# Kernel optimization log

Hardware: AMD Instinct MI355X
Metric: run time of the kernel (lower is better)

The kernel has to match this reference:

```python
import jax, jax.numpy as jnp
import numpy as np

B, D, E = 65536, 1024, 16
H1, H2 = 128, 64          # expert hidden dims (hidden_dim=128, hidden_dim//2)
R1, R2 = 64, 32           # router hidden dims
EPS = 1e-5                # BatchNorm eps


def setup_inputs() -> dict:
    key = jax.random.key(0)
    ks = jax.random.split(key, 16)
    s = 0.02
    inp = {
        "x": jax.random.normal(ks[0], (B, D), jnp.float32),
        # router BatchNorm1d (eval mode: running stats)
        "r_gamma": jnp.ones((D,), jnp.float32),
        "r_beta": jnp.zeros((D,), jnp.float32),
        "r_mean": jnp.zeros((D,), jnp.float32),
        "r_var": jnp.ones((D,), jnp.float32),
        # router MLP D->64->32->16
        "rW1": jax.random.normal(ks[1], (D, R1), jnp.float32) * s,
        "rb1": jnp.full((R1,), 0.1, jnp.float32),
        "rW2": jax.random.normal(ks[2], (R1, R2), jnp.float32) * s,
        "rb2": jnp.full((R2,), 0.1, jnp.float32),
        "rW3": jax.random.normal(ks[3], (R2, E), jnp.float32) * s,
        "rb3": jnp.full((E,), 0.1, jnp.float32),
        # per-expert BatchNorm1d (eval mode)
        "e_gamma": jnp.ones((E, D), jnp.float32),
        "e_beta": jnp.zeros((E, D), jnp.float32),
        "e_mean": jnp.zeros((E, D), jnp.float32),
        "e_var": jnp.ones((E, D), jnp.float32),
        # per-expert MLP D->128->64->1, stacked along expert dim
        "eW1": jax.random.normal(ks[4], (E, D, H1), jnp.float32) * s,
        "eb1": jnp.full((E, H1), 0.1, jnp.float32),
        "eW2": jax.random.normal(ks[5], (E, H1, H2), jnp.float32) * s,
        "eb2": jnp.full((E, H2), 0.1, jnp.float32),
        "eW3": jax.random.normal(ks[6], (E, H2, 1), jnp.float32) * s,
        "eb3": jnp.full((E, 1), 0.1, jnp.float32),
    }
    return inp


def reference(x, r_gamma, r_beta, r_mean, r_var, rW1, rb1, rW2, rb2, rW3, rb3,
              e_gamma, e_beta, e_mean, e_var, eW1, eb1, eW2, eb2, eW3, eb3):
    # ---- router: BN (eval) -> Linear/ReLU -> Linear/ReLU -> Linear -> softmax
    xn = (x - r_mean) * (r_gamma / jnp.sqrt(r_var + EPS)) + r_beta   # [B,D]
    h = jax.nn.relu(xn @ rW1 + rb1)
    h = jax.nn.relu(h @ rW2 + rb2)
    routing_weights = jax.nn.softmax(h @ rW3 + rb3, axis=1)          # [B,E]

    # ---- experts: fold per-expert BN into first linear to avoid [E,B,D] copy
    scale = e_gamma / jnp.sqrt(e_var + EPS)                          # [E,D]
    shift = e_beta - e_mean * scale                                  # [E,D]
    W1_eff = eW1 * scale[:, :, None]                                 # [E,D,H1]
    b1_eff = eb1 + jnp.einsum('ed,edh->eh', shift, eW1)              # [E,H1]

    h1 = jax.nn.relu(jnp.einsum('bd,edh->ebh', x, W1_eff) + b1_eff[:, None, :])  # [E,B,H1]
    h2 = jax.nn.relu(jnp.einsum('ebh,ehk->ebk', h1, eW2) + eb2[:, None, :])      # [E,B,H2]
    logits = jnp.einsum('ebk,eko->ebo', h2, eW3) + eb3[:, None, :]               # [E,B,1]
    expert_outputs = jax.nn.sigmoid(logits[:, :, 0]).T               # [B,E]

    weighted_pred = jnp.sum(routing_weights * expert_outputs, axis=1)  # [B]
    return weighted_pred, routing_weights, expert_outputs
```

## Files before the change

### kernel.cpp

```cpp
#include <hip/hip_runtime.h>


typedef unsigned short u16;
typedef __attribute__((ext_vector_type(8))) short bf16x8;
typedef __attribute__((ext_vector_type(4))) float f32x4;
typedef __attribute__((ext_vector_type(8))) unsigned short u16x8;
typedef __attribute__((ext_vector_type(4))) unsigned short u16x4;

#define MFMA16(a, b, c) __builtin_amdgcn_mfma_f32_16x16x32_bf16(a, b, c, 0, 0, 0)

#define B_ROWS 65536
#define NE 16
#define EPS 1e-5f

#define SBAR() __builtin_amdgcn_s_barrier()
#define VMCNT(n)                                             \
    do {                                                     \
        asm volatile("s_waitcnt vmcnt(" #n ")" ::: "memory");\
        __builtin_amdgcn_sched_barrier(0);                   \
    } while (0)

__device__ inline u16 f2bf(float f) {
    union { float f; unsigned u; } c; c.f = f;
    unsigned u = c.u;
    return (u16)((u + 0x7fffu + ((u >> 16) & 1u)) >> 16);
}

__device__ inline void gload16(const u16* g, u16* s) {
    __builtin_amdgcn_global_load_lds(
        (const __attribute__((address_space(1))) unsigned int*)g,
        (__attribute__((address_space(3))) unsigned int*)s,
        16, 0, 0);
}


__device__ void body_prep_x(int blk, int tid, const float* __restrict__ x,
                            u16* __restrict__ xs_g, u16* __restrict__ lds) {
    int p = tid & 15, rloc = tid >> 4;
    int r_g = blk * 16 + rloc;
    int lb = p & 7;
    int swz = (rloc >> 1) & 3;
    const float* xrow = x + (size_t)r_g * 1024;
#pragma unroll
    for (int i = 0; i < 8; ++i) {
        int kc = 2 * i + (p >> 3);
        int c = kc * 64 + lb * 8;
        float4 f0 = *(const float4*)(xrow + c);
        float4 f1 = *(const float4*)(xrow + c + 4);
        u16x8 u;
        u[0] = f2bf(f0.x); u[1] = f2bf(f0.y); u[2] = f2bf(f0.z); u[3] = f2bf(f0.w);
        u[4] = f2bf(f1.x); u[5] = f2bf(f1.y); u[6] = f2bf(f1.z); u[7] = f2bf(f1.w);
        int s = c >> 5;
        int q = (c >> 3) & 3;
        *(u16x8*)&lds[s * 512 + rloc * 32 + ((q ^ swz) << 3)] = u;
    }
    __syncthreads();
    int rb = blk >> 4, m0 = (blk & 15) * 16;
    int lane = tid & 63, th = tid >> 6;
#pragma unroll
    for (int j = 0; j < 8; ++j) {
        int c = j * 4 + th;
        u16x8 v = *(const u16x8*)&lds[c * 512 + lane * 8];
        *(u16x8*)&xs_g[((size_t)(rb * 32 + c) << 13) + m0 * 32 + lane * 8] = v;
    }
}

__device__ void body_prep_w1s(int t, const float* __restrict__ eW1, const float* __restrict__ eg,
                              const float* __restrict__ ev, u16* __restrict__ w1s) {
    int qp = t & 3, h = (t >> 2) & 255, s = (t >> 10) & 31, nt = t >> 15;
    int q = qp ^ ((h >> 1) & 3);
    int e = nt * 2 + (h >> 7), hl = h & 127;
    int k0 = s * 32 + q * 8;
    u16x8 u;
#pragma unroll
    for (int j = 0; j < 8; ++j) {
        int d = k0 + j;
        float sc = eg[e * 1024 + d] * rsqrtf(ev[e * 1024 + d] + EPS);
        u[j] = f2bf(eW1[((size_t)e * 1024 + d) * 128 + hl] * sc);
    }
    *(u16x8*)&w1s[((size_t)(nt * 32 + s) << 13) + h * 32 + qp * 8] = u;
}

__device__ void body_prep_b1(int g, int lane, const float* __restrict__ eW1,
                             const float* __restrict__ eg, const float* __restrict__ eb,
                             const float* __restrict__ em, const float* __restrict__ ev,
                             const float* __restrict__ eb1, float* __restrict__ b1e) {
    int e = g >> 7, h = g & 127;
    float s = 0.f;
    for (int d = lane; d < 1024; d += 64) {
        float sc = eg[e * 1024 + d] * rsqrtf(ev[e * 1024 + d] + EPS);
        float sh = eb[e * 1024 + d] - em[e * 1024 + d] * sc;
        s += sh * eW1[((size_t)e * 1024 + d) * 128 + h];
    }
#pragma unroll
    for (int m = 1; m < 64; m <<= 1) s += __shfl_xor(s, m, 64);
    if (lane == 0) b1e[e * 128 + h] = eb1[e * 128 + h] + s;
}

__device__ void body_prep_rw1s(int t, const float* __restrict__ rW1, const float* __restrict__ rg,
                               const float* __restrict__ rv, u16* __restrict__ rw1s) {
    int qp = t & 3, jj = (t >> 2) & 63, s = t >> 8;
    int q = qp ^ ((jj >> 1) & 3);
    int k0 = s * 32 + q * 8;
    u16x8 u;
#pragma unroll
    for (int k = 0; k < 8; ++k) {
        int d = k0 + k;
        float sc = rg[d] * rsqrtf(rv[d] + EPS);
        u[k] = f2bf(rW1[d * 64 + jj] * sc);
    }
    *(u16x8*)&rw1s[(s << 11) + jj * 32 + qp * 8] = u;
}

__device__ void body_prep_rb1(int j, int lane, const float* __restrict__ rW1,
                              const float* __restrict__ rg, const float* __restrict__ rbta,
                              const float* __restrict__ rm, const float* __restrict__ rv,
                              const float* __restrict__ rb1, float* __restrict__ rb1e) {
    float s = 0.f;
    for (int d = lane; d < 1024; d += 64) {
        float sc = rg[d] * rsqrtf(rv[d] + EPS);
        float sh = rbta[d] - rm[d] * sc;
        s += sh * rW1[d * 64 + j];
    }
#pragma unroll
    for (int m = 1; m < 64; m <<= 1) s += __shfl_xor(s, m, 64);
    if (lane == 0) rb1e[j] = rb1[j] + s;
}

__device__ void body_prep_w2s(int t, const float* __restrict__ eW2, u16* __restrict__ w2s) {
    int p = t & 15, j = (t >> 4) & 63, e = t >> 10;
    int lb = p ^ (j & 7);
    int h0 = lb * 8;
    u16x8 u;
#pragma unroll
    for (int jj = 0; jj < 8; ++jj)
        u[jj] = f2bf(eW2[((size_t)e * 128 + h0 + jj) * 64 + j]);
    *(u16x8*)&w2s[((e * 64 + j) << 7) + p * 8] = u;
}

__global__ __launch_bounds__(256) void prep_all(
    const float* __restrict__ x, u16* __restrict__ xs_g,
    const float* __restrict__ eW1, const float* __restrict__ eg,
    const float* __restrict__ eb, const float* __restrict__ em,
    const float* __restrict__ ev, const float* __restrict__ eb1,
    u16* __restrict__ w1s, float* __restrict__ b1e,
    const float* __restrict__ rW1, const float* __restrict__ rg,
    const float* __restrict__ rbta, const float* __restrict__ rm,
    const float* __restrict__ rv, const float* __restrict__ rb1,
    u16* __restrict__ rw1s, float* __restrict__ rb1e,
    const float* __restrict__ eW2, u16* __restrict__ w2s) {
    __shared__ __align__(16) u16 lds[16384];
    int bid = blockIdx.x, tid = threadIdx.x;
    if (bid < 4096) {
        body_prep_x(bid, tid, x, xs_g, lds);
    } else if (bid < 5120) {
        body_prep_w1s((bid - 4096) * 256 + tid, eW1, eg, ev, w1s);
    } else if (bid < 5632) {
        body_prep_b1((bid - 5120) * 4 + (tid >> 6), tid & 63, eW1, eg, eb, em, ev, eb1, b1e);
    } else if (bid < 5664) {
        body_prep_rw1s((bid - 5632) * 256 + tid, rW1, rg, rv, rw1s);
    } else if (bid < 5680) {
        body_prep_rb1((bid - 5664) * 4 + (tid >> 6), tid & 63, rW1, rg, rbta, rm, rv, rb1, rb1e);
    } else {
        body_prep_w2s((bid - 5680) * 256 + tid, eW2, w2s);
    }
}

__global__ __launch_bounds__(512, 2) void fused_main(
    const u16* __restrict__ xs_g, const u16* __restrict__ w1s,
    const float* __restrict__ b1e, const u16* __restrict__ w2s,
    const float* __restrict__ eb2, const float* __restrict__ eW3,
    const float* __restrict__ eb3, float* __restrict__ out_eo,
    const u16* __restrict__ rw1s, const float* __restrict__ rb1e,
    const float* __restrict__ rW2, const float* __restrict__ rb2,
    const float* __restrict__ rW3, const float* __restrict__ rb3,
    float* __restrict__ out_rw) {
    __shared__ __align__(16) char smem[131072];

    int tid = threadIdx.x;
    int wave = tid >> 6, lane = tid & 63, quad = lane >> 4, l15 = lane & 15;
    int phq = (quad ^ ((l15 >> 1) & 3)) * 8;

    if (blockIdx.x >= 256) {
        int i = blockIdx.x - 256;
        int rb = (i & 7) * 32 + ((i >> 3) >> 3);
        int nt = (i >> 3) & 7;
        int wm = wave >> 2, wn = wave & 3;

        u16* ring = (u16*)smem;
        const u16* gA = w1s + ((size_t)nt << 18);
        const u16* gB = xs_g + ((size_t)rb << 18);

        f32x4 acc[8][4] = {};

        auto STAGE = [&](int t) {
            u16* ls = ring + (t & 3) * 16384 + wave * 1024;
            const u16* ga = gA + (t << 13) + wave * 1024;
            const u16* gb = gB + (t << 13) + wave * 1024;
            gload16(ga + lane * 8, ls);
            gload16(ga + 512 + lane * 8, ls + 512);
            gload16(gb + lane * 8, ls + 8192);
            gload16(gb + 512 + lane * 8, ls + 8192 + 512);
        };
        auto COMPUTE = [&](int t) {
            const u16* lA = ring + (t & 3) * 16384;
            const u16* lB = lA + 8192;
            bf16x8 a[8], b[4];
#pragma unroll
            for (int ii = 0; ii < 8; ++ii)
                a[ii] = *(const bf16x8*)&lA[(wm * 128 + ii * 16 + l15) * 32 + phq];
#pragma unroll
            for (int jj = 0; jj < 4; ++jj)
                b[jj] = *(const bf16x8*)&lB[(wn * 64 + jj * 16 + l15) * 32 + phq];
            __builtin_amdgcn_s_setprio(1);
#pragma unroll
            for (int ii = 0; ii < 8; ++ii)
#pragma unroll
                for (int jj = 0; jj < 4; ++jj)
                    acc[ii][jj] = MFMA16(a[ii], b[jj], acc[ii][jj]);
            __builtin_amdgcn_s_setprio(0);
        };

        STAGE(0); STAGE(1); STAGE(2);
#pragma clang loop unroll(disable)
        for (int s = 0; s < 29; ++s) {
            SBAR();
            STAGE(s + 3);
            VMCNT(12);
            SBAR();
            COMPUTE(s);
        }
        SBAR(); VMCNT(8); SBAR(); COMPUTE(29);
        SBAR(); VMCNT(4); SBAR(); COMPUTE(30);
        SBAR(); VMCNT(0); SBAR(); COMPUTE(31);

        int e = nt * 2 + wm;
        u16* h1 = ring;
        SBAR();
#pragma unroll
        for (int ii = 0; ii < 8; ++ii) {
            float4 bv = *(const float4*)&b1e[e * 128 + ii * 16 + quad * 4];
            float bva[4] = {bv.x, bv.y, bv.z, bv.w};
            int h0 = wm * 128 + ii * 16 + quad * 4;
            int oc = h0 >> 3, hin = h0 & 7;
#pragma unroll
            for (int jj = 0; jj < 4; ++jj) {
                int m = wn * 64 + jj * 16 + l15;
                u16x4 pk;
#pragma unroll
                for (int r = 0; r < 4; ++r)
                    pk[r] = f2bf(fmaxf(acc[ii][jj][r] + bva[r], 0.f));
                int poc = (oc & 24) | ((oc ^ m) & 7);
                *(u16x4*)&h1[m * 256 + poc * 8 + hin] = pk;
            }
        }
        bf16x8 w2f[4][4];
        const u16* gW2 = w2s + e * 8192;
#pragma unroll
        for (int ks = 0; ks < 4; ++ks)
#pragma unroll
            for (int tj = 0; tj < 4; ++tj) {
                int jc = tj * 16 + l15;
                int pq = (ks * 4 + quad) ^ (jc & 7);
                w2f[ks][tj] = *(const bf16x8*)&gW2[jc * 128 + pq * 8];
            }
        asm volatile("s_waitcnt lgkmcnt(0)" ::: "memory");
        __builtin_amdgcn_sched_barrier(0);
        SBAR();

        f32x4 acc2[4][4] = {};
#pragma unroll
        for (int ks = 0; ks < 4; ++ks) {
            bf16x8 a2[4];
#pragma unroll
            for (int mi = 0; mi < 4; ++mi) {
                int m = wn * 64 + mi * 16 + l15;
                int oc2 = wm * 16 + ks * 4 + quad;
                int poc2 = (oc2 & 24) | ((oc2 ^ m) & 7);
                a2[mi] = *(const bf16x8*)&h1[m * 256 + poc2 * 8];
            }
#pragma unroll
            for (int mi = 0; mi < 4; ++mi)
#pragma unroll
                for (int tj = 0; tj < 4; ++tj)
                    acc2[mi][tj] = MFMA16(a2[mi], w2f[ks][tj], acc2[mi][tj]);
        }

        float b2v[4], w3v[4];
#pragma unroll
        for (int tj = 0; tj < 4; ++tj) {
            int jc = tj * 16 + l15;
            b2v[tj] = eb2[e * 64 + jc];
            w3v[tj] = eW3[e * 64 + jc];
        }
        float be3 = eb3[e];
#pragma unroll
        for (int mi = 0; mi < 4; ++mi) {
            float sv[4] = {0.f, 0.f, 0.f, 0.f};
#pragma unroll
            for (int tj = 0; tj < 4; ++tj)
#pragma unroll
                for (int r = 0; r < 4; ++r)
                    sv[r] += fmaxf(acc2[mi][tj][r] + b2v[tj], 0.f) * w3v[tj];
#pragma unroll
            for (int mask = 1; mask < 16; mask <<= 1)
#pragma unroll
                for (int r = 0; r < 4; ++r) sv[r] += __shfl_xor(sv[r], mask, 64);
            if (l15 == 0) {
#pragma unroll
                for (int r = 0; r < 4; ++r) {
                    int m = wn * 64 + mi * 16 + quad * 4 + r;
                    float z = sv[r] + be3;
                    out_eo[(size_t)(rb * 256 + m) * 16 + e] = 1.f / (1.f + __expf(-z));
                }
            }
        }
    } else {
        int rb = blockIdx.x;
        u16* ldsX = (u16*)smem;
        u16* ldsW = (u16*)smem + 16384;
        float* h_r = (float*)smem;
        float* h2s = (float*)(smem + 69632);
        const u16* gB = xs_g + ((size_t)rb << 18);

        f32x4 accr[4][2] = {};
        for (int kt = 0; kt < 16; ++kt) {
            const u16* gx = gB + ((size_t)(2 * kt) << 13) + wave * 1024;
            const u16* gw = rw1s + ((2 * kt) << 11) + wave * 512;
            u16* lx = ldsX + wave * 1024;
            gload16(gx + lane * 8, lx);
            gload16(gx + 512 + lane * 8, lx + 512);
            gload16(gx + 8192 + lane * 8, lx + 8192);
            gload16(gx + 8192 + 512 + lane * 8, lx + 8192 + 512);
            gload16(gw + lane * 8, ldsW + wave * 512);
            __syncthreads();
#pragma unroll
            for (int st = 0; st < 2; ++st) {
                bf16x8 aw[4], bx[2];
#pragma unroll
                for (int jf = 0; jf < 4; ++jf)
                    aw[jf] = *(const bf16x8*)&ldsW[st * 2048 + (jf * 16 + l15) * 32 + phq];
#pragma unroll
                for (int mf = 0; mf < 2; ++mf)
                    bx[mf] = *(const bf16x8*)&ldsX[st * 8192 + (wave * 32 + mf * 16 + l15) * 32 + phq];
#pragma unroll
                for (int jf = 0; jf < 4; ++jf)
#pragma unroll
                    for (int mf = 0; mf < 2; ++mf)
                        accr[jf][mf] = MFMA16(aw[jf], bx[mf], accr[jf][mf]);
            }
            __syncthreads();
        }

#pragma unroll
        for (int jf = 0; jf < 4; ++jf) {
            int j0 = jf * 16 + quad * 4;
            float4 bv = *(const float4*)&rb1e[j0];
#pragma unroll
            for (int mf = 0; mf < 2; ++mf) {
                int m = wave * 32 + mf * 16 + l15;
                float4 hv;
                hv.x = fmaxf(accr[jf][mf][0] + bv.x, 0.f);
                hv.y = fmaxf(accr[jf][mf][1] + bv.y, 0.f);
                hv.z = fmaxf(accr[jf][mf][2] + bv.z, 0.f);
                hv.w = fmaxf(accr[jf][mf][3] + bv.w, 0.f);
                *(float4*)&h_r[m * 68 + j0] = hv;
            }
        }
        __syncthreads();

        {
            int m = tid & 255, qg = tid >> 8;
            float h2r[16];
#pragma unroll
            for (int k = 0; k < 16; ++k) h2r[k] = 0.f;
            for (int i2 = 0; i2 < 64; ++i2) {
                float hv = h_r[m * 68 + i2];
                const float4* wrow = (const float4*)&rW2[i2 * 32 + qg * 16];
                float w[16];
                *(float4*)&w[0] = wrow[0];
                *(float4*)&w[4] = wrow[1];
                *(float4*)&w[8] = wrow[2];
                *(float4*)&w[12] = wrow[3];
#pragma unroll
                for (int k = 0; k < 16; ++k) h2r[k] += hv * w[k];
            }
#pragma unroll
            for (int k = 0; k < 16; ++k)
                h2r[k] = fmaxf(h2r[k] + rb2[qg * 16 + k], 0.f);
#pragma unroll
            for (int k = 0; k < 16; k += 4)
                *(float4*)&h2s[m * 36 + qg * 16 + k] = *(float4*)&h2r[k];
        }
        __syncthreads();

        if (tid < 256) {
            int mm = tid;
            float lg[16];
#pragma unroll
            for (int o = 0; o < 16; ++o) lg[o] = 0.f;
            for (int q = 0; q < 32; ++q) {
                float hv = h2s[mm * 36 + q];
                const float4* wr = (const float4*)&rW3[q * 16];
                float w[16];
                *(float4*)&w[0] = wr[0];
                *(float4*)&w[4] = wr[1];
                *(float4*)&w[8] = wr[2];
                *(float4*)&w[12] = wr[3];
#pragma unroll
                for (int o = 0; o < 16; ++o) lg[o] += hv * w[o];
            }
#pragma unroll
            for (int o = 0; o < 16; ++o) lg[o] += rb3[o];
            float mx = lg[0];
#pragma unroll
            for (int o = 1; o < 16; ++o) mx = fmaxf(mx, lg[o]);
            float ss = 0.f;
#pragma unroll
            for (int o = 0; o < 16; ++o) { lg[o] = __expf(lg[o] - mx); ss += lg[o]; }
            float inv = 1.f / ss;
            size_t base = (size_t)(rb * 256 + mm) * 16;
#pragma unroll
            for (int o = 0; o < 16; o += 4) {
                float4 v;
                v.x = lg[o] * inv; v.y = lg[o + 1] * inv;
                v.z = lg[o + 2] * inv; v.w = lg[o + 3] * inv;
                *(float4*)&out_rw[base + o] = v;
            }
        }
    }
}

__global__ void combine_kernel(const float* __restrict__ rw, const float* __restrict__ eo,
                               float* __restrict__ wp) {
    int b = blockIdx.x * 256 + threadIdx.x;
    const float4* r4 = (const float4*)(rw + (size_t)b * 16);
    const float4* o4 = (const float4*)(eo + (size_t)b * 16);
    float s = 0.f;
#pragma unroll
    for (int k = 0; k < 4; ++k) {
        float4 r = r4[k], o = o4[k];
        s += r.x * o.x + r.y * o.y + r.z * o.z + r.w * o.w;
    }
    wp[b] = s;
}


extern "C" void kernel_launch(void* const* d_in, const int* in_sizes, int n_in,
                              void* d_out, int out_size, void* d_ws, size_t ws_size,
                              hipStream_t stream) {
    const float* x       = (const float*)d_in[0];
    const float* r_gamma = (const float*)d_in[1];
    const float* r_beta  = (const float*)d_in[2];
    const float* r_mean  = (const float*)d_in[3];
    const float* r_var   = (const float*)d_in[4];
    const float* rW1     = (const float*)d_in[5];
    const float* rb1     = (const float*)d_in[6];
    const float* rW2     = (const float*)d_in[7];
    const float* rb2     = (const float*)d_in[8];
    const float* rW3     = (const float*)d_in[9];
    const float* rb3     = (const float*)d_in[10];
    const float* e_gamma = (const float*)d_in[11];
    const float* e_beta  = (const float*)d_in[12];
    const float* e_mean  = (const float*)d_in[13];
    const float* e_var   = (const float*)d_in[14];
    const float* eW1     = (const float*)d_in[15];
    const float* eb1     = (const float*)d_in[16];
    const float* eW2     = (const float*)d_in[17];
    const float* eb2     = (const float*)d_in[18];
    const float* eW3     = (const float*)d_in[19];
    const float* eb3     = (const float*)d_in[20];

    char* ws = (char*)d_ws;
    u16* xs_g   = (u16*)ws;
    u16* w1s    = (u16*)(ws + 134217728);
    u16* rw1s   = (u16*)(ws + 138412032);
    u16* w2s    = (u16*)(ws + 138543104);
    float* b1e  = (float*)(ws + 138805248);
    float* rb1e = (float*)(ws + 138813440);

    float* out_wp = (float*)d_out;
    float* out_rw = out_wp + B_ROWS;
    float* out_eo = out_rw + (size_t)B_ROWS * NE;

    prep_all<<<5744, 256, 0, stream>>>(
        x, xs_g,
        eW1, e_gamma, e_beta, e_mean, e_var, eb1, w1s, b1e,
        rW1, r_gamma, r_beta, r_mean, r_var, rb1, rw1s, rb1e,
        eW2, w2s);

    fused_main<<<2304, 512, 0, stream>>>(
        xs_g, w1s, b1e, w2s, eb2, eW3, eb3, out_eo,
        rw1s, rb1e, rW2, rb2, rW3, rb3, out_rw);

    combine_kernel<<<256, 256, 0, stream>>>(out_rw, out_eo, out_wp);
}
```

Before: 731.3 us.

## Use row-major bf16 operands and double-buffer MFMA fragments in expert GEMM loop

The prep kernel now writes x and the folded W1 matrices as plain row-major bf16, replacing the pre-tiled, swizzled layouts, which removes the LDS transpose pass in x prep. The main kernel gathers 32-wide K slices straight from the row-major arrays and drops the XOR swizzle on LDS reads. The K loop is restructured so register fragments for the next stage load while the current stage's MFMAs run (ping-pong fa0/fa1), and it waits with a different vmcnt. Dropping the swizzle risks LDS bank conflicts, and the strided global gathers may coalesce less well.

After: 748.8 us. 1.02x slower.

```diff
diff --git a/kernel.cpp b/kernel.cpp
--- a/kernel.cpp
+++ b/kernel.cpp
@@ -35,50 +35,32 @@
 
 
 __device__ void body_prep_x(int blk, int tid, const float* __restrict__ x,
-                            u16* __restrict__ xs_g, u16* __restrict__ lds) {
-    int p = tid & 15, rloc = tid >> 4;
-    int r_g = blk * 16 + rloc;
-    int lb = p & 7;
-    int swz = (rloc >> 1) & 3;
-    const float* xrow = x + (size_t)r_g * 1024;
+                            u16* __restrict__ xbf) {
 #pragma unroll
     for (int i = 0; i < 8; ++i) {
-        int kc = 2 * i + (p >> 3);
-        int c = kc * 64 + lb * 8;
-        float4 f0 = *(const float4*)(xrow + c);
-        float4 f1 = *(const float4*)(xrow + c + 4);
+        size_t fi = (((size_t)blk * 2048) + i * 256 + tid) * 8;
+        float4 f0 = *(const float4*)(x + fi);
+        float4 f1 = *(const float4*)(x + fi + 4);
         u16x8 u;
         u[0] = f2bf(f0.x); u[1] = f2bf(f0.y); u[2] = f2bf(f0.z); u[3] = f2bf(f0.w);
         u[4] = f2bf(f1.x); u[5] = f2bf(f1.y); u[6] = f2bf(f1.z); u[7] = f2bf(f1.w);
-        int s = c >> 5;
-        int q = (c >> 3) & 3;
-        *(u16x8*)&lds[s * 512 + rloc * 32 + ((q ^ swz) << 3)] = u;
-    }
-    __syncthreads();
-    int rb = blk >> 4, m0 = (blk & 15) * 16;
-    int lane = tid & 63, th = tid >> 6;
+        *(u16x8*)&xbf[fi] = u;
+    }
+}
+
+__device__ void body_prep_w1s(int t, const float* __restrict__ eW1, const float* __restrict__ eg,
+                              const float* __restrict__ ev, u16* __restrict__ w1sr) {
+    int ko = t & 127, h = t >> 7;
+    int nt = h >> 8, sub = h & 255;
+    int e = nt * 2 + (sub >> 7), hl = sub & 127;
+    u16x8 u;
 #pragma unroll
     for (int j = 0; j < 8; ++j) {
-        int c = j * 4 + th;
-        u16x8 v = *(const u16x8*)&lds[c * 512 + lane * 8];
-        *(u16x8*)&xs_g[((size_t)(rb * 32 + c) << 13) + m0 * 32 + lane * 8] = v;
-    }
-}
-
-__device__ void body_prep_w1s(int t, const float* __restrict__ eW1, const float* __restrict__ eg,
-                              const float* __restrict__ ev, u16* __restrict__ w1s) {
-    int qp = t & 3, h = (t >> 2) & 255, s = (t >> 10) & 31, nt = t >> 15;
-    int q = qp ^ ((h >> 1) & 3);
-    int e = nt * 2 + (h >> 7), hl = h & 127;
-    int k0 = s * 32 + q * 8;
-    u16x8 u;
-#pragma unroll
-    for (int j = 0; j < 8; ++j) {
-        int d = k0 + j;
+        int d = ko * 8 + j;
         float sc = eg[e * 1024 + d] * rsqrtf(ev[e * 1024 + d] + EPS);
         u[j] = f2bf(eW1[((size_t)e * 1024 + d) * 128 + hl] * sc);
     }
-    *(u16x8*)&w1s[((size_t)(nt * 32 + s) << 13) + h * 32 + qp * 8] = u;
+    *(u16x8*)&w1sr[((size_t)h << 10) + ko * 8] = u;
 }
 
 __device__ void body_prep_b1(int g, int lane, const float* __restrict__ eW1,
@@ -98,18 +80,16 @@
 }
 
 __device__ void body_prep_rw1s(int t, const float* __restrict__ rW1, const float* __restrict__ rg,
-                               const float* __restrict__ rv, u16* __restrict__ rw1s) {
-    int qp = t & 3, jj = (t >> 2) & 63, s = t >> 8;
-    int q = qp ^ ((jj >> 1) & 3);
-    int k0 = s * 32 + q * 8;
+                               const float* __restrict__ rv, u16* __restrict__ rw1sr) {
+    int ko = t & 127, j = t >> 7;
     u16x8 u;
 #pragma unroll
     for (int k = 0; k < 8; ++k) {
-        int d = k0 + k;
+        int d = ko * 8 + k;
         float sc = rg[d] * rsqrtf(rv[d] + EPS);
-        u[k] = f2bf(rW1[d * 64 + jj] * sc);
-    }
-    *(u16x8*)&rw1s[(s << 11) + jj * 32 + qp * 8] = u;
+        u[k] = f2bf(rW1[d * 64 + j] * sc);
+    }
+    *(u16x8*)&rw1sr[(j << 10) + ko * 8] = u;
 }
 
 __device__ void body_prep_rb1(int j, int lane, const float* __restrict__ rW1,
@@ -139,26 +119,25 @@
 }
 
 __global__ __launch_bounds__(256) void prep_all(
-    const float* __restrict__ x, u16* __restrict__ xs_g,
+    const float* __restrict__ x, u16* __restrict__ xbf,
     const float* __restrict__ eW1, const float* __restrict__ eg,
     const float* __restrict__ eb, const float* __restrict__ em,
     const float* __restrict__ ev, const float* __restrict__ eb1,
-    u16* __restrict__ w1s, float* __restrict__ b1e,
+    u16* __restrict__ w1sr, float* __restrict__ b1e,
     const float* __restrict__ rW1, const float* __restrict__ rg,
     const float* __restrict__ rbta, const float* __restrict__ rm,
     const float* __restrict__ rv, const float* __restrict__ rb1,
-    u16* __restrict__ rw1s, float* __restrict__ rb1e,
+    u16* __restrict__ rw1sr, float* __restrict__ rb1e,
     const float* __restrict__ eW2, u16* __restrict__ w2s) {
-    __shared__ __align__(16) u16 lds[16384];
     int bid = blockIdx.x, tid = threadIdx.x;
     if (bid < 4096) {
-        body_prep_x(bid, tid, x, xs_g, lds);
+        body_prep_x(bid, tid, x, xbf);
     } else if (bid < 5120) {
-        body_prep_w1s((bid - 4096) * 256 + tid, eW1, eg, ev, w1s);
+        body_prep_w1s((bid - 4096) * 256 + tid, eW1, eg, ev, w1sr);
     } else if (bid < 5632) {
         body_prep_b1((bid - 5120) * 4 + (tid >> 6), tid & 63, eW1, eg, eb, em, ev, eb1, b1e);
     } else if (bid < 5664) {
-        body_prep_rw1s((bid - 5632) * 256 + tid, rW1, rg, rv, rw1s);
+        body_prep_rw1s((bid - 5632) * 256 + tid, rW1, rg, rv, rw1sr);
     } else if (bid < 5680) {
         body_prep_rb1((bid - 5664) * 4 + (tid >> 6), tid & 63, rW1, rg, rbta, rm, rv, rb1, rb1e);
     } else {
@@ -167,11 +146,11 @@
 }
 
 __global__ __launch_bounds__(512, 2) void fused_main(
-    const u16* __restrict__ xs_g, const u16* __restrict__ w1s,
+    const u16* __restrict__ xbf, const u16* __restrict__ w1sr,
     const float* __restrict__ b1e, const u16* __restrict__ w2s,
     const float* __restrict__ eb2, const float* __restrict__ eW3,
     const float* __restrict__ eb3, float* __restrict__ out_eo,
-    const u16* __restrict__ rw1s, const float* __restrict__ rb1e,
+    const u16* __restrict__ rw1sr, const float* __restrict__ rb1e,
     const float* __restrict__ rW2, const float* __restrict__ rb2,
     const float* __restrict__ rW3, const float* __restrict__ rb3,
     float* __restrict__ out_rw) {
@@ -179,60 +158,89 @@
 
     int tid = threadIdx.x;
     int wave = tid >> 6, lane = tid & 63, quad = lane >> 4, l15 = lane & 15;
-    int phq = (quad ^ ((l15 >> 1) & 3)) * 8;
+    int lr = lane >> 2, lc = lane & 3;
 
     if (blockIdx.x >= 256) {
         int i = blockIdx.x - 256;
-        int rb = (i & 7) * 32 + ((i >> 3) >> 3);
+        int rb = (i & 7) * 32 + (i >> 6);
         int nt = (i >> 3) & 7;
         int wm = wave >> 2, wn = wave & 3;
 
         u16* ring = (u16*)smem;
-        const u16* gA = w1s + ((size_t)nt << 18);
-        const u16* gB = xs_g + ((size_t)rb << 18);
+        const u16* gA0 = w1sr + ((size_t)(nt * 256 + wave * 32 + lr) << 10) + lc * 8;
+        const u16* gB0 = xbf + ((size_t)(rb * 256 + wave * 32 + lr) << 10) + lc * 8;
+        int laneA = (wm * 128 + l15) * 32 + quad * 8;
+        int laneB = (wn * 64 + l15) * 32 + quad * 8;
 
         f32x4 acc[8][4] = {};
+        bf16x8 fa0[8], fb0[4], fa1[8], fb1[4];
 
         auto STAGE = [&](int t) {
             u16* ls = ring + (t & 3) * 16384 + wave * 1024;
-            const u16* ga = gA + (t << 13) + wave * 1024;
-            const u16* gb = gB + (t << 13) + wave * 1024;
-            gload16(ga + lane * 8, ls);
-            gload16(ga + 512 + lane * 8, ls + 512);
-            gload16(gb + lane * 8, ls + 8192);
-            gload16(gb + 512 + lane * 8, ls + 8192 + 512);
+            const u16* ga = gA0 + t * 32;
+            const u16* gb = gB0 + t * 32;
+            gload16(ga, ls);
+            gload16(ga + 16384, ls + 512);
+            gload16(gb, ls + 8192);
+            gload16(gb + 16384, ls + 8192 + 512);
         };
-        auto COMPUTE = [&](int t) {
+        auto LOADFRAG = [&](bf16x8 (&fa)[8], bf16x8 (&fb)[4], int t) {
             const u16* lA = ring + (t & 3) * 16384;
-            const u16* lB = lA + 8192;
-            bf16x8 a[8], b[4];
 #pragma unroll
             for (int ii = 0; ii < 8; ++ii)
-                a[ii] = *(const bf16x8*)&lA[(wm * 128 + ii * 16 + l15) * 32 + phq];
+                fa[ii] = *(const bf16x8*)&lA[laneA + ii * 512];
 #pragma unroll
             for (int jj = 0; jj < 4; ++jj)
-                b[jj] = *(const bf16x8*)&lB[(wn * 64 + jj * 16 + l15) * 32 + phq];
+                fb[jj] = *(const bf16x8*)&lA[8192 + laneB + jj * 512];
+        };
+        auto MFMACL = [&](bf16x8 (&fa)[8], bf16x8 (&fb)[4]) {
             __builtin_amdgcn_s_setprio(1);
 #pragma unroll
             for (int ii = 0; ii < 8; ++ii)
 #pragma unroll
                 for (int jj = 0; jj < 4; ++jj)
-                    acc[ii][jj] = MFMA16(a[ii], b[jj], acc[ii][jj]);
+                    acc[ii][jj] = MFMA16(fa[ii], fb[jj], acc[ii][jj]);
             __builtin_amdgcn_s_setprio(0);
         };
 
+#define BODY(S, CA, CB, NA, NB)                    \
+    do {                                           \
+        SBAR();                                    \
+        STAGE((S) + 3);                            \
+        VMCNT(8);                                  \
+        SBAR();                                    \
+        __builtin_amdgcn_sched_barrier(0);         \
+        LOADFRAG(NA, NB, (S) + 1);                 \
+        __builtin_amdgcn_sched_barrier(0);         \
+        MFMACL(CA, CB);                            \
+    } while (0)
+
         STAGE(0); STAGE(1); STAGE(2);
+        VMCNT(8);
+        SBAR();
+        __builtin_amdgcn_sched_barrier(0);
+        LOADFRAG(fa0, fb0, 0);
+
 #pragma clang loop unroll(disable)
-        for (int s = 0; s < 29; ++s) {
-            SBAR();
-            STAGE(s + 3);
-            VMCNT(12);
-            SBAR();
-            COMPUTE(s);
-        }
-        SBAR(); VMCNT(8); SBAR(); COMPUTE(29);
-        SBAR(); VMCNT(4); SBAR(); COMPUTE(30);
-        SBAR(); VMCNT(0); SBAR(); COMPUTE(31);
+        for (int s2 = 0; s2 < 28; s2 += 2) {
+            BODY(s2, fa0, fb0, fa1, fb1);
+            BODY(s2 + 1, fa1, fb1, fa0, fb0);
+        }
+        BODY(28, fa0, fb0, fa1, fb1);
+        VMCNT(4);
+        SBAR();
+        __builtin_amdgcn_sched_barrier(0);
+        LOADFRAG(fa0, fb0, 30);
+        __builtin_amdgcn_sched_barrier(0);
+        MFMACL(fa1, fb1);
+        VMCNT(0);
+        SBAR();
+        __builtin_amdgcn_sched_barrier(0);
+        LOADFRAG(fa1, fb1, 31);
+        __builtin_amdgcn_sched_barrier(0);
+        MFMACL(fa0, fb0);
+        MFMACL(fa1, fb1);
+#undef BODY
 
         int e = nt * 2 + wm;
         u16* h1 = ring;
@@ -321,28 +329,29 @@
         u16* ldsW = (u16*)smem + 16384;
         float* h_r = (float*)smem;
         float* h2s = (float*)(smem + 69632);
-        const u16* gB = xs_g + ((size_t)rb << 18);
+        const u16* gX0 = xbf + ((size_t)(rb * 256 + wave * 32 + lr) << 10) + lc * 8;
+        int stw = wave >> 2, q3 = wave & 3;
+        const u16* gW0 = rw1sr + ((size_t)(q3 * 16 + lr) << 10) + lc * 8;
 
         f32x4 accr[4][2] = {};
         for (int kt = 0; kt < 16; ++kt) {
-            const u16* gx = gB + ((size_t)(2 * kt) << 13) + wave * 1024;
-            const u16* gw = rw1s + ((2 * kt) << 11) + wave * 512;
+            int s0 = kt * 2;
             u16* lx = ldsX + wave * 1024;
-            gload16(gx + lane * 8, lx);
-            gload16(gx + 512 + lane * 8, lx + 512);
-            gload16(gx + 8192 + lane * 8, lx + 8192);
-            gload16(gx + 8192 + 512 + lane * 8, lx + 8192 + 512);
-            gload16(gw + lane * 8, ldsW + wave * 512);
+            gload16(gX0 + s0 * 32, lx);
+            gload16(gX0 + 16384 + s0 * 32, lx + 512);
+            gload16(gX0 + (s0 + 1) * 32, lx + 8192);
+            gload16(gX0 + 16384 + (s0 + 1) * 32, lx + 8192 + 512);
+            gload16(gW0 + (s0 + stw) * 32, ldsW + stw * 2048 + q3 * 512);
             __syncthreads();
 #pragma unroll
             for (int st = 0; st < 2; ++st) {
                 bf16x8 aw[4], bx[2];
 #pragma unroll
                 for (int jf = 0; jf < 4; ++jf)
-                    aw[jf] = *(const bf16x8*)&ldsW[st * 2048 + (jf * 16 + l15) * 32 + phq];
+                    aw[jf] = *(const bf16x8*)&ldsW[st * 2048 + (jf * 16 + l15) * 32 + quad * 8];
 #pragma unroll
                 for (int mf = 0; mf < 2; ++mf)
-                    bx[mf] = *(const bf16x8*)&ldsX[st * 8192 + (wave * 32 + mf * 16 + l15) * 32 + phq];
+                    bx[mf] = *(const bf16x8*)&ldsX[st * 8192 + (wave * 32 + mf * 16 + l15) * 32 + quad * 8];
 #pragma unroll
                 for (int jf = 0; jf < 4; ++jf)
 #pragma unroll
@@ -472,9 +481,9 @@
     const float* eb3     = (const float*)d_in[20];
 
     char* ws = (char*)d_ws;
-    u16* xs_g   = (u16*)ws;
-    u16* w1s    = (u16*)(ws + 134217728);
-    u16* rw1s   = (u16*)(ws + 138412032);
+    u16* xbf    = (u16*)ws;
+    u16* w1sr   = (u16*)(ws + 134217728);
+    u16* rw1sr  = (u16*)(ws + 138412032);
     u16* w2s    = (u16*)(ws + 138543104);
     float* b1e  = (float*)(ws + 138805248);
     float* rb1e = (float*)(ws + 138813440);
@@ -484,14 +493,14 @@
     float* out_eo = out_rw + (size_t)B_ROWS * NE;
 
     prep_all<<<5744, 256, 0, stream>>>(
-        x, xs_g,
-        eW1, e_gamma, e_beta, e_mean, e_var, eb1, w1s, b1e,
-        rW1, r_gamma, r_beta, r_mean, r_var, rb1, rw1s, rb1e,
+        x, xbf,
+        eW1, e_gamma, e_beta, e_mean, e_var, eb1, w1sr, b1e,
+        rW1, r_gamma, r_beta, r_mean, r_var, rb1, rw1sr, rb1e,
         eW2, w2s);
 
     fused_main<<<2304, 512, 0, stream>>>(
-        xs_g, w1s, b1e, w2s, eb2, eW3, eb3, out_eo,
-        rw1s, rb1e, rW2, rb2, rW3, rb3, out_rw);
+        xbf, w1sr, b1e, w2s, eb2, eW3, eb3, out_eo,
+        rw1sr, rb1e, rW2, rb2, rW3, rb3, out_rw);
 
     combine_kernel<<<256, 256, 0, stream>>>(out_rw, out_eo, out_wp);
 }
```
